# Optimization experiments

Hardware: AMD Instinct MI355X
Metric: run time of the kernel (lower is better)

The kernel has to match this reference:

```python
import jax, jax.numpy as jnp
import numpy as np

N = 100_000      # nodes
E = 1_600_000    # directed edges (avg degree 16)
F_IN = 128       # num_node_features
H = 8            # heads in conv1
C = 32           # hidden_channels
G = 64           # graphs in batch
NC = 10          # num_classes


def setup_inputs() -> dict:
    key = jax.random.key(0)
    ks = jax.random.split(key, 12)
    gl = lambda k, shape, fan: (jax.random.normal(k, shape, jnp.float32) / np.sqrt(fan)).astype(jnp.float32)
    return {
        "x": jax.random.normal(ks[0], (N, F_IN), jnp.float32),
        "edge_index": jax.random.randint(ks[1], (2, E), 0, N, dtype=jnp.int32),
        "batch": jnp.sort(jax.random.randint(ks[2], (N,), 0, G, dtype=jnp.int32)),
        "W1": gl(ks[3], (F_IN, H * C), F_IN),
        "att_src1": gl(ks[4], (H, C), C),
        "att_dst1": gl(ks[5], (H, C), C),
        "b1": jnp.zeros((H * C,), jnp.float32),
        "W2": gl(ks[6], (H * C, C), H * C),
        "att_src2": gl(ks[7], (1, C), C),
        "att_dst2": gl(ks[8], (1, C), C),
        "b2": jnp.zeros((C,), jnp.float32),
        "Wlin": gl(ks[9], (C, NC), C),
        "blin": jnp.zeros((NC,), jnp.float32),
    }


def gat_conv(x, src, dst, W, att_src, att_dst, bias, heads, ch, concat):
    """PyG GATConv (eval mode): gather, LeakyReLU(0.2) scores, segment softmax over dst, scatter-sum."""
    n = x.shape[0]
    h = (x @ W).reshape(n, heads, ch)                     # [N,H,C]
    a_s = jnp.sum(h * att_src, axis=-1)                   # [N,H]
    a_d = jnp.sum(h * att_dst, axis=-1)                   # [N,H]
    e = jax.nn.leaky_relu(a_s[src] + a_d[dst], 0.2)       # [E,H]
    m = jax.ops.segment_max(e, dst, num_segments=n)       # [N,H], stable softmax
    p = jnp.exp(e - m[dst])
    z = jax.ops.segment_sum(p, dst, num_segments=n)
    coef = p / (z[dst] + 1e-16)                           # [E,H]
    out = jax.ops.segment_sum(coef[:, :, None] * h[src], dst, num_segments=n)  # [N,H,C]
    out = out.reshape(n, heads * ch) if concat else out.mean(axis=1)
    return out + bias


def reference(x, edge_index, batch, W1, att_src1, att_dst1, b1,
              W2, att_src2, att_dst2, b2, Wlin, blin):
    n = x.shape[0]
    loops = jnp.arange(n, dtype=edge_index.dtype)         # GATConv add_self_loops=True
    src = jnp.concatenate([edge_index[0], loops])
    dst = jnp.concatenate([edge_index[1], loops])

    h = gat_conv(x, src, dst, W1, att_src1, att_dst1, b1, H, C, concat=True)
    h = jax.nn.elu(h)                                     # dropout is identity in eval
    h = gat_conv(h, src, dst, W2, att_src2, att_dst2, b2, 1, C, concat=False)

    # global_mean_pool over graph ids
    sums = jax.ops.segment_sum(h, batch, num_segments=G)  # [G,C]
    cnts = jax.ops.segment_sum(jnp.ones((n,), h.dtype), batch, num_segments=G)
    pooled = sums / jnp.maximum(cnts, 1.0)[:, None]

    return pooled @ Wlin + blin                           # [G,NC]
```

## Files before the change

kernel.cpp:

```cpp
#include <hip/hip_runtime.h>
#include <cstdint>

#define NN 100000
#define EE 1600000
#define GG 64
#define FIN 128
#define HC 256
#define NC 10

typedef short v8s __attribute__((ext_vector_type(8)));
typedef float v4f __attribute__((ext_vector_type(4)));

static __device__ __forceinline__ float lrelu(float x) { return x > 0.f ? x : 0.2f * x; }
static __device__ __forceinline__ float bf2f(unsigned short b) {
  return __uint_as_float(((unsigned int)b) << 16);
}
static __device__ __forceinline__ unsigned short f2bf(float f) {
  unsigned int u = __float_as_uint(f);
  unsigned int r = (u + 0x7FFFu + ((u >> 16) & 1u)) >> 16;
  return (unsigned short)r;
}
static __device__ __forceinline__ void unpack2(unsigned int u, float& f0, float& f1) {
  f0 = __uint_as_float(u << 16);
  f1 = __uint_as_float(u & 0xFFFF0000u);
}

__global__ void k_zero(unsigned int* __restrict__ p, int n) {
  int i = blockIdx.x * 256 + threadIdx.x;
  if (i < n) p[i] = 0u;
}

__global__ void k_prep(const float* __restrict__ W1, unsigned short* __restrict__ W1tg) {
  const int b = blockIdx.x, t = threadIdx.x;
  if (t < 128) W1tg[b * 128 + t] = f2bf(W1[t * HC + b]);
}

__global__ __launch_bounds__(256) void k_gemm1(const float* __restrict__ x,
                                               const unsigned short* __restrict__ W1tg,
                                               const float* __restrict__ att_src1,
                                               const float* __restrict__ att_dst1,
                                               unsigned short* __restrict__ h1b,
                                               float* __restrict__ as1,
                                               float* __restrict__ ad1) {
  const int t = threadIdx.x;
  const int m0 = blockIdx.x * 64;
  const int n0 = blockIdx.y * 128;
  const int hb = blockIdx.y * 4;
  const int lane = t & 63;
  const int wm = t >> 6;
  const int ml = lane & 15;
  const int quad = lane >> 4;
  int row = m0 + wm * 16 + ml; if (row >= NN) row = NN - 1;
  v4f acc[8];
#pragma unroll
  for (int tt = 0; tt < 8; ++tt) acc[tt] = (v4f){0.f, 0.f, 0.f, 0.f};
#pragma unroll
  for (int kk = 0; kk < 4; ++kk) {
    const int k0 = kk * 32 + quad * 8;
    float4 lo = *(const float4*)(x + (size_t)row * FIN + k0);
    float4 hi = *(const float4*)(x + (size_t)row * FIN + k0 + 4);
    v8s a;
    a[0] = (short)f2bf(lo.x); a[1] = (short)f2bf(lo.y);
    a[2] = (short)f2bf(lo.z); a[3] = (short)f2bf(lo.w);
    a[4] = (short)f2bf(hi.x); a[5] = (short)f2bf(hi.y);
    a[6] = (short)f2bf(hi.z); a[7] = (short)f2bf(hi.w);
#pragma unroll
    for (int tt = 0; tt < 8; ++tt) {
      v8s b = *(const v8s*)(W1tg + (size_t)(n0 + tt * 16 + ml) * FIN + k0);
      acc[tt] = __builtin_amdgcn_mfma_f32_16x16x32_bf16(a, b, acc[tt], 0, 0, 0);
    }
  }
#pragma unroll
  for (int tt = 0; tt < 8; ++tt) {
#pragma unroll
    for (int r = 0; r < 4; ++r) {
      int rg = m0 + wm * 16 + quad * 4 + r;
      if (rg < NN) h1b[(size_t)rg * HC + n0 + tt * 16 + ml] = f2bf(acc[tt][r]);
    }
  }
  float ps[4][4], pd[4][4];
#pragma unroll
  for (int i = 0; i < 4; ++i)
#pragma unroll
    for (int r = 0; r < 4; ++r) { ps[i][r] = 0.f; pd[i][r] = 0.f; }
#pragma unroll
  for (int i = 0; i < 4; ++i) {
#pragma unroll
    for (int half = 0; half < 2; ++half) {
      const int tt = 2 * i + half;
      const float a_s = att_src1[(hb + i) * 32 + half * 16 + ml];
      const float a_d = att_dst1[(hb + i) * 32 + half * 16 + ml];
#pragma unroll
      for (int r = 0; r < 4; ++r) {
        ps[i][r] += acc[tt][r] * a_s;
        pd[i][r] += acc[tt][r] * a_d;
      }
    }
  }
#pragma unroll
  for (int i = 0; i < 4; ++i) {
#pragma unroll
    for (int r = 0; r < 4; ++r) {
      float s = ps[i][r], d = pd[i][r];
      s += __shfl_xor(s, 1, 64); s += __shfl_xor(s, 2, 64);
      s += __shfl_xor(s, 4, 64); s += __shfl_xor(s, 8, 64);
      d += __shfl_xor(d, 1, 64); d += __shfl_xor(d, 2, 64);
      d += __shfl_xor(d, 4, 64); d += __shfl_xor(d, 8, 64);
      ps[i][r] = s; pd[i][r] = d;
    }
  }
  if (ml == 0) {
#pragma unroll
    for (int r = 0; r < 4; ++r) {
      int rg = m0 + wm * 16 + quad * 4 + r;
      if (rg < NN) {
#pragma unroll
        for (int i = 0; i < 4; ++i) {
          as1[rg * 8 + hb + i] = ps[i][r];
          ad1[rg * 8 + hb + i] = pd[i][r];
        }
      }
    }
  }
}

__global__ void k_count(const int* __restrict__ ei, int* __restrict__ counts) {
  int e = blockIdx.x * 256 + threadIdx.x;
  if (e < EE) atomicAdd(&counts[ei[EE + e]], 1);
}

__global__ void k_scan1(const int* __restrict__ counts, int* __restrict__ offs,
                        int* __restrict__ bsums) {
  __shared__ int s[256];
  const int t = threadIdx.x;
  const int i = blockIdx.x * 256 + t;
  int v = (i < NN) ? counts[i] : 0;
  s[t] = v;
  __syncthreads();
  for (int off = 1; off < 256; off <<= 1) {
    int tv = (t >= off) ? s[t - off] : 0;
    __syncthreads();
    s[t] += tv;
    __syncthreads();
  }
  if (i < NN) offs[i] = s[t] - v;
  if (t == 255) bsums[blockIdx.x] = s[255];
}

__global__ void k_scan2(int* __restrict__ bsums, int nb) {
  __shared__ int s[512];
  const int t = threadIdx.x;
  int v = (t < nb) ? bsums[t] : 0;
  s[t] = v;
  __syncthreads();
  for (int off = 1; off < 512; off <<= 1) {
    int tv = (t >= off) ? s[t - off] : 0;
    __syncthreads();
    s[t] += tv;
    __syncthreads();
  }
  if (t < nb) bsums[t] = s[t] - v;
}

__global__ void k_scan3(int* __restrict__ offs, const int* __restrict__ bsums,
                        int* __restrict__ cursor) {
  const int i = blockIdx.x * 256 + threadIdx.x;
  if (i < NN) {
    int v = offs[i] + bsums[i >> 8];
    offs[i] = v;
    cursor[i] = v;
  }
  if (i == 0) offs[NN] = EE;
}

__global__ void k_scatter(const int* __restrict__ ei, int* __restrict__ cursor,
                          const float* __restrict__ as1, const float* __restrict__ ad1,
                          int* __restrict__ esrc, float* __restrict__ wt) {
  int e = blockIdx.x * 256 + threadIdx.x;
  if (e < EE) {
    int s = ei[e];
    int d = ei[EE + e];
    int p = atomicAdd(&cursor[d], 1);
    esrc[p] = s;
    float4 a0 = *(const float4*)(as1 + s * 8);
    float4 a1 = *(const float4*)(as1 + s * 8 + 4);
    float4 b0 = *(const float4*)(ad1 + d * 8);
    float4 b1 = *(const float4*)(ad1 + d * 8 + 4);
    float4 r0, r1;
    r0.x = __expf(lrelu(a0.x + b0.x)); r0.y = __expf(lrelu(a0.y + b0.y));
    r0.z = __expf(lrelu(a0.z + b0.z)); r0.w = __expf(lrelu(a0.w + b0.w));
    r1.x = __expf(lrelu(a1.x + b1.x)); r1.y = __expf(lrelu(a1.y + b1.y));
    r1.z = __expf(lrelu(a1.z + b1.z)); r1.w = __expf(lrelu(a1.w + b1.w));
    *(float4*)(wt + (size_t)p * 8) = r0;
    *(float4*)(wt + (size_t)p * 8 + 4) = r1;
  }
}

__global__ __launch_bounds__(128) void k_agg1(const unsigned short* __restrict__ h1b,
                                              const float* __restrict__ as1,
                                              const float* __restrict__ ad1,
                                              const int* __restrict__ offs,
                                              const int* __restrict__ esrc,
                                              const float* __restrict__ wt,
                                              const float* __restrict__ b1,
                                              const float* __restrict__ W2,
                                              const float* __restrict__ att_src2,
                                              const float* __restrict__ att_dst2,
                                              unsigned short* __restrict__ h2b,
                                              float* __restrict__ as2,
                                              float* __restrict__ ad2) {
  __shared__ float wl[2][32][8];
  __shared__ float sv[256];
  __shared__ float zsh[2][8];
  __shared__ float sp[4][33];
  const int t = threadIdx.x;
  const int lane = t & 63;
  const int w = t >> 6;
  const int head = lane >> 3;
  const int n0 = blockIdx.x * 2;
  const int o0 = offs[n0], o1 = offs[n0 + 1], o2 = offs[n0 + 2];
  const uint2* h1u2 = (const uint2*)h1b;

  int sreg[2] = {0, 0};
  const int cnt0 = min(32, o1 - o0);
  const int cnt1 = min(32, o2 - o1);
  if (lane < cnt0) sreg[0] = esrc[o0 + lane];
  if (lane < cnt1) sreg[1] = esrc[o1 + lane];
  {
    const int j = t >> 2, hh = (t & 3) * 2;
    if (j < cnt0) *(float2*)&wl[0][j][hh] = *(const float2*)(wt + (size_t)(o0 + j) * 8 + hh);
    if (j < cnt1) *(float2*)&wl[1][j][hh] = *(const float2*)(wt + (size_t)(o1 + j) * 8 + hh);
  }
  __syncthreads();

  for (int ns = 0; ns < 2; ++ns) {
    const int n = n0 + ns;
    const int sBeg = ns ? o1 : o0;
    const int sEnd = ns ? o2 : o1;
    float acc0 = 0.f, acc1 = 0.f, acc2 = 0.f, acc3 = 0.f, z = 0.f;
    if (w == 0) {
      float w0 = __expf(lrelu(as1[n * 8 + head] + ad1[n * 8 + head]));
      z = w0;
      uint2 q = h1u2[(size_t)n * 64 + lane];
      float f0, f1, f2, f3; unpack2(q.x, f0, f1); unpack2(q.y, f2, f3);
      acc0 = w0 * f0; acc1 = w0 * f1; acc2 = w0 * f2; acc3 = w0 * f3;
    }
    int sregc = sreg[ns];
    for (int base = sBeg; base < sEnd; base += 32) {
      const int cnt = min(32, sEnd - base);
      if (base != sBeg) {
        sregc = 0;
        if (lane < cnt) sregc = esrc[base + lane];
        __syncthreads();
        const int j = t >> 2, hh = (t & 3) * 2;
        if (j < cnt) *(float2*)&wl[ns][j][hh] = *(const float2*)(wt + (size_t)(base + j) * 8 + hh);
        __syncthreads();
      }
#pragma unroll 8
      for (int j2 = w; j2 < cnt; j2 += 2) {
        int sj = __builtin_amdgcn_readlane(sregc, j2);
        uint2 q = h1u2[(size_t)sj * 64 + lane];
        float wv = wl[ns][j2][head];
        float f0, f1, f2, f3; unpack2(q.x, f0, f1); unpack2(q.y, f2, f3);
        z += wv;
        acc0 += wv * f0; acc1 += wv * f1; acc2 += wv * f2; acc3 += wv * f3;
      }
    }

    __syncthreads();
    if (w == 0) {
      *(float4*)&sv[4 * lane] = make_float4(acc0, acc1, acc2, acc3);
      if ((lane & 7) == 0) zsh[0][head] = z;
    }
    __syncthreads();
    if (w == 1) {
      float4 p = *(float4*)&sv[4 * lane];
      p.x += acc0; p.y += acc1; p.z += acc2; p.w += acc3;
      *(float4*)&sv[4 * lane] = p;
      if ((lane & 7) == 0) zsh[1][head] = z;
    }
    __syncthreads();
    {
      const int ho = t >> 4;
      const float zf = zsh[0][ho] + zsh[1][ho];
      const float zi = 1.0f / (zf + 1e-16f);
      float2 bb = *(const float2*)(b1 + 2 * t);
      float v0 = sv[2 * t] * zi + bb.x;
      float v1 = sv[2 * t + 1] * zi + bb.y;
      v0 = v0 > 0.f ? v0 : (__expf(v0) - 1.0f);
      v1 = v1 > 0.f ? v1 : (__expf(v1) - 1.0f);
      __syncthreads();
      sv[2 * t] = v0; sv[2 * t + 1] = v1;
    }
    __syncthreads();
    const int c = t & 31, rr = t >> 5;
    const float* svp = sv + rr * 64;
    const float* w2p = W2 + rr * 64 * 32 + c;
    float p = 0.f;
#pragma unroll 16
    for (int kk = 0; kk < 64; ++kk) p += svp[kk] * w2p[kk * 32];
    sp[rr][c] = p;
    __syncthreads();
    if (t < 32) {
      float hv = sp[0][t] + sp[1][t] + sp[2][t] + sp[3][t];
      h2b[(size_t)n * 32 + t] = f2bf(hv);
      float ps = hv * att_src2[t];
      float pd = hv * att_dst2[t];
#pragma unroll
      for (int m = 16; m >= 1; m >>= 1) {
        ps += __shfl_xor(ps, m, 64);
        pd += __shfl_xor(pd, m, 64);
      }
      if (t == 0) { as2[n] = ps; ad2[n] = pd; }
    }
    __syncthreads();
  }
}

__global__ __launch_bounds__(256) void k_agg2(const unsigned short* __restrict__ h2b,
                                              const float* __restrict__ as2,
                                              const float* __restrict__ ad2,
                                              const int* __restrict__ offs,
                                              const int* __restrict__ esrc,
                                              const float* __restrict__ b2,
                                              float* __restrict__ h3) {
  const int t = threadIdx.x;
  const int g = t >> 5, c = t & 31;
  const int n = blockIdx.x * 8 + g;
  const int sbase = t & 32;
  const int start = offs[n], end = offs[n + 1];
  const float adn = ad2[n];
  float w0 = __expf(lrelu(as2[n] + adn));
  float z = w0;
  float acc = w0 * bf2f(h2b[(size_t)n * 32 + c]);
  for (int base = start; base < end; base += 32) {
    const int cnt = min(32, end - base);
    int s_reg = 0; float w_reg = 0.f;
    if (c < cnt) {
      s_reg = esrc[base + c];
      w_reg = __expf(lrelu(as2[s_reg] + adn));
    }
#pragma unroll 8
    for (int j = 0; j < cnt; ++j) {
      int sj = __shfl(s_reg, sbase + j, 64);
      float wj = __shfl(w_reg, sbase + j, 64);
      z += wj;
      acc += wj * bf2f(h2b[(size_t)sj * 32 + c]);
    }
  }
  h3[(size_t)n * 32 + c] = acc / (z + 1e-16f) + b2[c];
}

__global__ __launch_bounds__(256) void k_poolfin(const float* __restrict__ h3,
                                                 const int* __restrict__ batch,
                                                 const float* __restrict__ Wlin,
                                                 const float* __restrict__ blin,
                                                 float* __restrict__ out) {
  __shared__ int bounds[2];
  __shared__ float red[8][33];
  __shared__ float mean[32];
  const int g = blockIdx.x;
  const int t = threadIdx.x;
  if (t < 2) {
    int target = g + t;
    int lo = 0, hi = NN;
    while (lo < hi) { int mid = (lo + hi) >> 1; if (batch[mid] < target) lo = mid + 1; else hi = mid; }
    bounds[t] = lo;
  }
  __syncthreads();
  const int lo = bounds[0], hi = bounds[1];
  const int rr = t >> 5, c = t & 31;
  float a = 0.f;
  for (int r = lo + rr; r < hi; r += 8) a += h3[(size_t)r * 32 + c];
  red[rr][c] = a;
  __syncthreads();
  if (rr == 0) {
    float s = 0.f;
#pragma unroll
    for (int i = 0; i < 8; ++i) s += red[i][c];
    float ct = (float)(hi - lo);
    ct = ct > 1.f ? ct : 1.f;
    mean[c] = s / ct;
  }
  __syncthreads();
  if (t < NC) {
    float acc = 0.f;
#pragma unroll
    for (int cc = 0; cc < 32; ++cc) acc += mean[cc] * Wlin[cc * NC + t];
    out[g * NC + t] = acc + blin[t];
  }
}

extern "C" void kernel_launch(void* const* d_in, const int* in_sizes, int n_in,
                              void* d_out, int out_size, void* d_ws, size_t ws_size,
                              hipStream_t stream) {
  const float* x        = (const float*)d_in[0];
  const int*   ei       = (const int*)d_in[1];
  const int*   batch    = (const int*)d_in[2];
  const float* W1       = (const float*)d_in[3];
  const float* att_src1 = (const float*)d_in[4];
  const float* att_dst1 = (const float*)d_in[5];
  const float* b1       = (const float*)d_in[6];
  const float* W2       = (const float*)d_in[7];
  const float* att_src2 = (const float*)d_in[8];
  const float* att_dst2 = (const float*)d_in[9];
  const float* b2       = (const float*)d_in[10];
  const float* Wlin     = (const float*)d_in[11];
  const float* blin     = (const float*)d_in[12];
  float* out = (float*)d_out;
  char* ws = (char*)d_ws;

  unsigned short* h1b  = (unsigned short*)(ws + 0);
  float* as1    = (float*)(ws + 51200000);
  float* ad1    = (float*)(ws + 54400000);
  int* counts   = (int*)(ws + 57600000);
  int* offs     = (int*)(ws + 58000000);
  int* cursor   = (int*)(ws + 58400256);
  int* esrc     = (int*)(ws + 58800256);
  int* bsums    = (int*)(ws + 65200256);
  unsigned short* h2b = (unsigned short*)(ws + 65202048);
  float* as2    = (float*)(ws + 71602048);
  float* ad2    = (float*)(ws + 72002048);
  unsigned short* W1tg = (unsigned short*)(ws + 72402048);
  float* wt     = (float*)(ws + 72467584);
  float* h3     = (float*)(ws + 72467584);

  const int nb_scan = (NN + 255) / 256;

  k_zero<<<nb_scan, 256, 0, stream>>>((unsigned int*)counts, NN);
  k_prep<<<256, 128, 0, stream>>>(W1, W1tg);

  dim3 g1((NN + 63) / 64, 2);
  k_gemm1<<<g1, 256, 0, stream>>>(x, W1tg, att_src1, att_dst1, h1b, as1, ad1);

  k_count<<<(EE + 255) / 256, 256, 0, stream>>>(ei, counts);
  k_scan1<<<nb_scan, 256, 0, stream>>>(counts, offs, bsums);
  k_scan2<<<1, 512, 0, stream>>>(bsums, nb_scan);
  k_scan3<<<nb_scan, 256, 0, stream>>>(offs, bsums, cursor);
  k_scatter<<<(EE + 255) / 256, 256, 0, stream>>>(ei, cursor, as1, ad1, esrc, wt);

  k_agg1<<<NN / 2, 128, 0, stream>>>(h1b, as1, ad1, offs, esrc, wt, b1, W2,
                                     att_src2, att_dst2, h2b, as2, ad2);

  k_agg2<<<NN / 8, 256, 0, stream>>>(h2b, as2, ad2, offs, esrc, b2, h3);
  k_poolfin<<<GG, 256, 0, stream>>>(h3, batch, Wlin, blin, out);
}
```

Measured before the change: 690.0 us.

## Pre-convert x to bf16, store edge weights as bf16, restructure agg2

Adds a pass that converts x to bf16 once (fused with zeroing counts) so gemm1 loads bf16 directly, which halves gemm1's x reads but adds a separate full read and write pass over x. Edge softmax weights are now stored as packed bf16 (16 bytes per edge instead of 32), reducing scatter writes and agg1 reads at the cost of weight precision. k_agg2 is rewritten to one node per wavefront, with 4 edge slots of 16 lanes each loading two packed bf16 columns and a cross-lane reduction at the end. This aims for wider loads and more memory-level parallelism per node.

```diff
diff --git a/kernel.cpp b/kernel.cpp
--- a/kernel.cpp
+++ b/kernel.cpp
@@ -20,14 +20,24 @@
   unsigned int r = (u + 0x7FFFu + ((u >> 16) & 1u)) >> 16;
   return (unsigned short)r;
 }
+static __device__ __forceinline__ unsigned int pk2bf(float a, float b) {
+  return (unsigned int)f2bf(a) | ((unsigned int)f2bf(b) << 16);
+}
 static __device__ __forceinline__ void unpack2(unsigned int u, float& f0, float& f1) {
   f0 = __uint_as_float(u << 16);
   f1 = __uint_as_float(u & 0xFFFF0000u);
 }
 
-__global__ void k_zero(unsigned int* __restrict__ p, int n) {
-  int i = blockIdx.x * 256 + threadIdx.x;
-  if (i < n) p[i] = 0u;
+__global__ __launch_bounds__(256) void k_prepx(const float* __restrict__ x,
+                                               unsigned short* __restrict__ xb,
+                                               unsigned int* __restrict__ counts) {
+  const int idx = blockIdx.x * 256 + threadIdx.x;
+  const int i4 = idx * 4;
+  float4 v = *(const float4*)(x + i4);
+  ushort4 u;
+  u.x = f2bf(v.x); u.y = f2bf(v.y); u.z = f2bf(v.z); u.w = f2bf(v.w);
+  *(ushort4*)(xb + i4) = u;
+  if (idx < NN) counts[idx] = 0u;
 }
 
 __global__ void k_prep(const float* __restrict__ W1, unsigned short* __restrict__ W1tg) {
@@ -35,7 +45,7 @@
   if (t < 128) W1tg[b * 128 + t] = f2bf(W1[t * HC + b]);
 }
 
-__global__ __launch_bounds__(256) void k_gemm1(const float* __restrict__ x,
+__global__ __launch_bounds__(256) void k_gemm1(const unsigned short* __restrict__ xb,
                                                const unsigned short* __restrict__ W1tg,
                                                const float* __restrict__ att_src1,
                                                const float* __restrict__ att_dst1,
@@ -57,13 +67,7 @@
 #pragma unroll
   for (int kk = 0; kk < 4; ++kk) {
     const int k0 = kk * 32 + quad * 8;
-    float4 lo = *(const float4*)(x + (size_t)row * FIN + k0);
-    float4 hi = *(const float4*)(x + (size_t)row * FIN + k0 + 4);
-    v8s a;
-    a[0] = (short)f2bf(lo.x); a[1] = (short)f2bf(lo.y);
-    a[2] = (short)f2bf(lo.z); a[3] = (short)f2bf(lo.w);
-    a[4] = (short)f2bf(hi.x); a[5] = (short)f2bf(hi.y);
-    a[6] = (short)f2bf(hi.z); a[7] = (short)f2bf(hi.w);
+    v8s a = *(const v8s*)(xb + (size_t)row * FIN + k0);
 #pragma unroll
     for (int tt = 0; tt < 8; ++tt) {
       v8s b = *(const v8s*)(W1tg + (size_t)(n0 + tt * 16 + ml) * FIN + k0);
@@ -175,7 +179,7 @@
 
 __global__ void k_scatter(const int* __restrict__ ei, int* __restrict__ cursor,
                           const float* __restrict__ as1, const float* __restrict__ ad1,
-                          int* __restrict__ esrc, float* __restrict__ wt) {
+                          int* __restrict__ esrc, uint4* __restrict__ wt16) {
   int e = blockIdx.x * 256 + threadIdx.x;
   if (e < EE) {
     int s = ei[e];
@@ -186,13 +190,12 @@
     float4 a1 = *(const float4*)(as1 + s * 8 + 4);
     float4 b0 = *(const float4*)(ad1 + d * 8);
     float4 b1 = *(const float4*)(ad1 + d * 8 + 4);
-    float4 r0, r1;
-    r0.x = __expf(lrelu(a0.x + b0.x)); r0.y = __expf(lrelu(a0.y + b0.y));
-    r0.z = __expf(lrelu(a0.z + b0.z)); r0.w = __expf(lrelu(a0.w + b0.w));
-    r1.x = __expf(lrelu(a1.x + b1.x)); r1.y = __expf(lrelu(a1.y + b1.y));
-    r1.z = __expf(lrelu(a1.z + b1.z)); r1.w = __expf(lrelu(a1.w + b1.w));
-    *(float4*)(wt + (size_t)p * 8) = r0;
-    *(float4*)(wt + (size_t)p * 8 + 4) = r1;
+    uint4 u;
+    u.x = pk2bf(__expf(lrelu(a0.x + b0.x)), __expf(lrelu(a0.y + b0.y)));
+    u.y = pk2bf(__expf(lrelu(a0.z + b0.z)), __expf(lrelu(a0.w + b0.w)));
+    u.z = pk2bf(__expf(lrelu(a1.x + b1.x)), __expf(lrelu(a1.y + b1.y)));
+    u.w = pk2bf(__expf(lrelu(a1.z + b1.z)), __expf(lrelu(a1.w + b1.w)));
+    wt16[p] = u;
   }
 }
 
@@ -201,7 +204,7 @@
                                               const float* __restrict__ ad1,
                                               const int* __restrict__ offs,
                                               const int* __restrict__ esrc,
-                                              const float* __restrict__ wt,
+                                              const unsigned int* __restrict__ wt4,
                                               const float* __restrict__ b1,
                                               const float* __restrict__ W2,
                                               const float* __restrict__ att_src2,
@@ -227,9 +230,15 @@
   if (lane < cnt0) sreg[0] = esrc[o0 + lane];
   if (lane < cnt1) sreg[1] = esrc[o1 + lane];
   {
-    const int j = t >> 2, hh = (t & 3) * 2;
-    if (j < cnt0) *(float2*)&wl[0][j][hh] = *(const float2*)(wt + (size_t)(o0 + j) * 8 + hh);
-    if (j < cnt1) *(float2*)&wl[1][j][hh] = *(const float2*)(wt + (size_t)(o1 + j) * 8 + hh);
+    const int j = t >> 2, hq = t & 3;
+    if (j < cnt0) {
+      float f0, f1; unpack2(wt4[(size_t)(o0 + j) * 4 + hq], f0, f1);
+      *(float2*)&wl[0][j][hq * 2] = make_float2(f0, f1);
+    }
+    if (j < cnt1) {
+      float f0, f1; unpack2(wt4[(size_t)(o1 + j) * 4 + hq], f0, f1);
+      *(float2*)&wl[1][j][hq * 2] = make_float2(f0, f1);
+    }
   }
   __syncthreads();
 
@@ -252,8 +261,11 @@
         sregc = 0;
         if (lane < cnt) sregc = esrc[base + lane];
         __syncthreads();
-        const int j = t >> 2, hh = (t & 3) * 2;
-        if (j < cnt) *(float2*)&wl[ns][j][hh] = *(const float2*)(wt + (size_t)(base + j) * 8 + hh);
+        const int j = t >> 2, hq = t & 3;
+        if (j < cnt) {
+          float f0, f1; unpack2(wt4[(size_t)(base + j) * 4 + hq], f0, f1);
+          *(float2*)&wl[ns][j][hq * 2] = make_float2(f0, f1);
+        }
         __syncthreads();
       }
 #pragma unroll 8
@@ -325,30 +337,52 @@
                                               const float* __restrict__ b2,
                                               float* __restrict__ h3) {
   const int t = threadIdx.x;
-  const int g = t >> 5, c = t & 31;
-  const int n = blockIdx.x * 8 + g;
-  const int sbase = t & 32;
+  const int lane = t & 63;
+  const int wv = t >> 6;
+  const int n = blockIdx.x * 4 + wv;
+  const int col = lane & 15;
+  const int slot = lane >> 4;
+  const unsigned int* h2u = (const unsigned int*)h2b;
   const int start = offs[n], end = offs[n + 1];
   const float adn = ad2[n];
-  float w0 = __expf(lrelu(as2[n] + adn));
-  float z = w0;
-  float acc = w0 * bf2f(h2b[(size_t)n * 32 + c]);
-  for (int base = start; base < end; base += 32) {
-    const int cnt = min(32, end - base);
-    int s_reg = 0; float w_reg = 0.f;
-    if (c < cnt) {
-      s_reg = esrc[base + c];
-      w_reg = __expf(lrelu(as2[s_reg] + adn));
-    }
-#pragma unroll 8
-    for (int j = 0; j < cnt; ++j) {
-      int sj = __shfl(s_reg, sbase + j, 64);
-      float wj = __shfl(w_reg, sbase + j, 64);
-      z += wj;
-      acc += wj * bf2f(h2b[(size_t)sj * 32 + c]);
-    }
-  }
-  h3[(size_t)n * 32 + c] = acc / (z + 1e-16f) + b2[c];
+  float z = 0.f, acc0 = 0.f, acc1 = 0.f;
+  if (slot == 0) {
+    float w0 = __expf(lrelu(as2[n] + adn));
+    unsigned int q = h2u[(size_t)n * 16 + col];
+    float f0, f1; unpack2(q, f0, f1);
+    z = w0; acc0 = w0 * f0; acc1 = w0 * f1;
+  }
+  for (int base = start; base < end; base += 64) {
+    const int cnt = min(64, end - base);
+    int sreg = 0; float wreg = 0.f;
+    if (lane < cnt) {
+      sreg = esrc[base + lane];
+      wreg = __expf(lrelu(as2[sreg] + adn));
+    }
+    const int jmax = (cnt + 3) >> 2;
+#pragma unroll 4
+    for (int j = 0; j < jmax; ++j) {
+      const int e = 4 * j + slot;
+      int sj = __shfl(sreg, e, 64);
+      float wj = __shfl(wreg, e, 64);
+      if (e < cnt) {
+        unsigned int q = h2u[(size_t)sj * 16 + col];
+        float f0, f1; unpack2(q, f0, f1);
+        z += wj; acc0 += wj * f0; acc1 += wj * f1;
+      }
+    }
+  }
+  acc0 += __shfl_xor(acc0, 16, 64); acc0 += __shfl_xor(acc0, 32, 64);
+  acc1 += __shfl_xor(acc1, 16, 64); acc1 += __shfl_xor(acc1, 32, 64);
+  z    += __shfl_xor(z, 16, 64);    z    += __shfl_xor(z, 32, 64);
+  if (slot == 0) {
+    const float zi = 1.0f / (z + 1e-16f);
+    float2 bb = *(const float2*)(b2 + 2 * col);
+    float2 o;
+    o.x = acc0 * zi + bb.x;
+    o.y = acc1 * zi + bb.y;
+    *(float2*)(h3 + (size_t)n * 32 + 2 * col) = o;
+  }
 }
 
 __global__ __launch_bounds__(256) void k_poolfin(const float* __restrict__ h3,
@@ -411,37 +445,38 @@
   char* ws = (char*)d_ws;
 
   unsigned short* h1b  = (unsigned short*)(ws + 0);
-  float* as1    = (float*)(ws + 51200000);
-  float* ad1    = (float*)(ws + 54400000);
-  int* counts   = (int*)(ws + 57600000);
-  int* offs     = (int*)(ws + 58000000);
-  int* cursor   = (int*)(ws + 58400256);
-  int* esrc     = (int*)(ws + 58800256);
-  int* bsums    = (int*)(ws + 65200256);
-  unsigned short* h2b = (unsigned short*)(ws + 65202048);
-  float* as2    = (float*)(ws + 71602048);
-  float* ad2    = (float*)(ws + 72002048);
-  unsigned short* W1tg = (unsigned short*)(ws + 72402048);
-  float* wt     = (float*)(ws + 72467584);
-  float* h3     = (float*)(ws + 72467584);
+  unsigned short* xb   = (unsigned short*)(ws + 51200000);
+  float* as1    = (float*)(ws + 76800000);
+  float* ad1    = (float*)(ws + 80000000);
+  int* counts   = (int*)(ws + 83200000);
+  int* offs     = (int*)(ws + 83600000);
+  int* cursor   = (int*)(ws + 84000256);
+  int* esrc     = (int*)(ws + 84400256);
+  int* bsums    = (int*)(ws + 90800256);
+  unsigned short* h2b = (unsigned short*)(ws + 90802048);
+  float* as2    = (float*)(ws + 97202048);
+  float* ad2    = (float*)(ws + 97602048);
+  unsigned short* W1tg = (unsigned short*)(ws + 98002048);
+  uint4* wt16   = (uint4*)(ws + 98067584);
+  float* h3     = (float*)(ws + 98067584);
 
   const int nb_scan = (NN + 255) / 256;
 
-  k_zero<<<nb_scan, 256, 0, stream>>>((unsigned int*)counts, NN);
+  k_prepx<<<12500, 256, 0, stream>>>(x, xb, (unsigned int*)counts);
   k_prep<<<256, 128, 0, stream>>>(W1, W1tg);
 
   dim3 g1((NN + 63) / 64, 2);
-  k_gemm1<<<g1, 256, 0, stream>>>(x, W1tg, att_src1, att_dst1, h1b, as1, ad1);
+  k_gemm1<<<g1, 256, 0, stream>>>(xb, W1tg, att_src1, att_dst1, h1b, as1, ad1);
 
   k_count<<<(EE + 255) / 256, 256, 0, stream>>>(ei, counts);
   k_scan1<<<nb_scan, 256, 0, stream>>>(counts, offs, bsums);
   k_scan2<<<1, 512, 0, stream>>>(bsums, nb_scan);
   k_scan3<<<nb_scan, 256, 0, stream>>>(offs, bsums, cursor);
-  k_scatter<<<(EE + 255) / 256, 256, 0, stream>>>(ei, cursor, as1, ad1, esrc, wt);
-
-  k_agg1<<<NN / 2, 128, 0, stream>>>(h1b, as1, ad1, offs, esrc, wt, b1, W2,
-                                     att_src2, att_dst2, h2b, as2, ad2);
-
-  k_agg2<<<NN / 8, 256, 0, stream>>>(h2b, as2, ad2, offs, esrc, b2, h3);
+  k_scatter<<<(EE + 255) / 256, 256, 0, stream>>>(ei, cursor, as1, ad1, esrc, wt16);
+
+  k_agg1<<<NN / 2, 128, 0, stream>>>(h1b, as1, ad1, offs, esrc, (const unsigned int*)wt16,
+                                     b1, W2, att_src2, att_dst2, h2b, as2, ad2);
+
+  k_agg2<<<NN / 4, 256, 0, stream>>>(h2b, as2, ad2, offs, esrc, b2, h3);
   k_poolfin<<<GG, 256, 0, stream>>>(h3, batch, Wlin, blin, out);
 }
```

New measurement: 667.4 us. -3.3%, faster.
